# Optimization experiments

Measured on AMD Instinct MI355X. Metric: run time of the kernel, lower is better.

## Reference

```python
import jax, jax.numpy as jnp
import numpy as np

NHEADS = 16
LN_EPS = 1e-5


def setup_inputs() -> dict:
    key = jax.random.key(0)
    ks = jax.random.split(key, 12)
    B, L, D = 8, 1024, 1024
    bound = 1.0 / np.sqrt(D)
    inp = {
        'query': jax.random.normal(ks[0], (B, L, D), jnp.float32),
        'key':   jax.random.normal(ks[1], (B, L, D), jnp.float32),
        'value': jax.random.normal(ks[2], (B, L, D), jnp.float32),
        'q_mask': jnp.ones((B, L), jnp.float32),
        'k_mask': jnp.ones((B, L), jnp.float32),
        'Wq': jax.random.uniform(ks[3], (D, D), jnp.float32, -bound, bound),
        'bq': jax.random.uniform(ks[4], (D,), jnp.float32, -bound, bound),
        'Wk': jax.random.uniform(ks[5], (D, D), jnp.float32, -bound, bound),
        'bk': jax.random.uniform(ks[6], (D,), jnp.float32, -bound, bound),
        'Wv': jax.random.uniform(ks[7], (D, D), jnp.float32, -bound, bound),
        'bv': jax.random.uniform(ks[8], (D,), jnp.float32, -bound, bound),
        'Wo': jax.random.uniform(ks[9], (D, D), jnp.float32, -bound, bound),
        'bo': jax.random.uniform(ks[10], (D,), jnp.float32, -bound, bound),
        'gamma': jnp.ones((D,), jnp.float32),
        'beta': jnp.zeros((D,), jnp.float32),
    }
    return inp


def reference(query, key, value, q_mask, k_mask, Wq, bq, Wk, bk, Wv, bv, Wo, bo, gamma, beta):
    B, L, D = query.shape
    H = NHEADS
    d = D // H
    residual = query
    # linear projections (torch Linear: x @ W.T + b)
    q = query @ Wq.T + bq
    k = key @ Wk.T + bk
    v = value @ Wv.T + bv
    # NOTE: module does a raw contiguous view [B, L, H*d] -> [B*H, L, d]
    # (NOT a transpose-based head split). Replicate exactly.
    q = q.reshape(B * H, L, d)
    k = k.reshape(B * H, L, d)
    v = v.reshape(B * H, L, d)
    # masks tiled head-major: repeat(nheads, 1) -> [H*B, L]
    qm = jnp.tile(q_mask, (H, 1))
    km = jnp.tile(k_mask, (H, 1))
    mask = qm[:, :, None] * km[:, None, :]  # [B*H, L, L] outer product
    scores = jnp.einsum('bqd,bkd->bqk', q, k) / np.sqrt(d).astype(np.float32)
    A = jnp.exp(jnp.where(mask == 0, -jnp.inf, scores))  # unstable exp, as in source
    A_sum = jnp.clip(jnp.sum(A, axis=-1, keepdims=True), 2e-15, None)
    attn = A / A_sum
    context = (attn @ v).reshape(B, L, H * d)
    out = context @ Wo.T + bo
    # dropout is identity in eval mode
    x = residual + out
    mean = jnp.mean(x, axis=-1, keepdims=True)
    var = jnp.mean(jnp.square(x - mean), axis=-1, keepdims=True)
    return (x - mean) / jnp.sqrt(var + LN_EPS) * gamma + beta
```

## Files before the change

kernel.cpp:

```cpp
#include <hip/hip_runtime.h>
#include <hip/hip_bf16.h>


typedef __bf16 bf16x8 __attribute__((ext_vector_type(8)));
typedef float  f32x4  __attribute__((ext_vector_type(4)));

#define KK 1024
#define NN 1024

union BfPack4 { __bf16 h[4]; uint2 u; };
union BfPack8 { __bf16 h[8]; uint4 u; };

__device__ __forceinline__ void lds_copy16(void* lds, const void* gsrc) {
  __builtin_amdgcn_global_load_lds(
      (__attribute__((address_space(1))) void*)(uintptr_t)gsrc,
      (__attribute__((address_space(3))) void*)(unsigned int)(uintptr_t)lds,
      16, 0, 0);
}

struct Cvt4 { const float* src[4]; __bf16* dst; };

__global__ __launch_bounds__(256) void cvt_w(Cvt4 a) {
  const int z = blockIdx.y;
  const float* s = a.src[z];
  __bf16* d = a.dst + (size_t)z * (KK * NN);
  const int i = (blockIdx.x * 256 + threadIdx.x) * 4;
  float4 f = *(const float4*)&s[i];
  BfPack4 p;
  p.h[0] = (__bf16)f.x; p.h[1] = (__bf16)f.y;
  p.h[2] = (__bf16)f.z; p.h[3] = (__bf16)f.w;
  *(uint2*)&d[i] = p.u;
}

struct Cvt3 { const float* src[3]; __bf16* dst; };

__global__ __launch_bounds__(256) void cvt_a(Cvt3 a) {
  const int z = blockIdx.y;
  const float* s = a.src[z];
  __bf16* d = a.dst + (size_t)z * ((size_t)8 << 20);
  const size_t i = ((size_t)blockIdx.x * 256 + threadIdx.x) * 8;
  float4 f0 = *(const float4*)&s[i];
  float4 f1 = *(const float4*)&s[i + 4];
  BfPack8 p;
  p.h[0] = (__bf16)f0.x; p.h[1] = (__bf16)f0.y;
  p.h[2] = (__bf16)f0.z; p.h[3] = (__bf16)f0.w;
  p.h[4] = (__bf16)f1.x; p.h[5] = (__bf16)f1.y;
  p.h[6] = (__bf16)f1.z; p.h[7] = (__bf16)f1.w;
  *(uint4*)&d[i] = p.u;
}

struct G8 {
  const __bf16* A[3];
  const __bf16* W[3];
  const float*  bias[3];
  void*         C[3];
};

#define BAR()   __builtin_amdgcn_s_barrier()
#define PRIO(x) __builtin_amdgcn_s_setprio(x)
#define WAIT_LGKM0() do { asm volatile("s_waitcnt lgkmcnt(0)" ::: "memory"); \
                          __builtin_amdgcn_sched_barrier(0); } while (0)
#define WAIT_VM4()  asm volatile("s_waitcnt vmcnt(4)" ::: "memory")
#define WAIT_VM0()  asm volatile("s_waitcnt vmcnt(0)" ::: "memory")

#define STAGE_A(buf, half, kt) do {                                          \
  lds_copy16(smem + (buf)*32768 + (half)*16384 + ldsW,                       \
             pA0[half] + (size_t)(kt)*64);                                   \
  lds_copy16(smem + (buf)*32768 + (half)*16384 + ldsW + 1024,                \
             pA1[half] + (size_t)(kt)*64); } while (0)

#define STAGE_B(buf, half, kt) do {                                          \
  lds_copy16(smem + 65536 + (buf)*32768 + (half)*16384 + ldsW,               \
             pB0[half] + (size_t)(kt)*64);                                   \
  lds_copy16(smem + 65536 + (buf)*32768 + (half)*16384 + ldsW + 1024,        \
             pB1[half] + (size_t)(kt)*64); } while (0)

#define LDA(buf, mh) do {                                                    \
  const char* _p = aSelf + (buf)*32768 + (mh)*8192;                          \
  _Pragma("unroll") for (int i_ = 0; i_ < 4; ++i_) {                         \
    af[i_][0] = *(const bf16x8*)(_p + i_*2048 + c0_);                        \
    af[i_][1] = *(const bf16x8*)(_p + i_*2048 + c1_); } } while (0)

#define LDB(buf, nh) do {                                                    \
  const char* _p = bSelf + (buf)*32768 + (nh)*4096;                          \
  _Pragma("unroll") for (int j_ = 0; j_ < 2; ++j_) {                         \
    bf[(nh)*2 + j_][0] = *(const bf16x8*)(_p + j_*2048 + c0_);               \
    bf[(nh)*2 + j_][1] = *(const bf16x8*)(_p + j_*2048 + c1_); } } while (0)

#define MM(mh, nh) do {                                                      \
  _Pragma("unroll") for (int i_ = 0; i_ < 4; ++i_)                           \
  _Pragma("unroll") for (int j_ = 0; j_ < 2; ++j_) {                         \
    acc[(mh)*4+i_][(nh)*2+j_] = __builtin_amdgcn_mfma_f32_16x16x32_bf16(     \
        af[i_][0], bf[(nh)*2+j_][0], acc[(mh)*4+i_][(nh)*2+j_], 0, 0, 0);    \
    acc[(mh)*4+i_][(nh)*2+j_] = __builtin_amdgcn_mfma_f32_16x16x32_bf16(     \
        af[i_][1], bf[(nh)*2+j_][1], acc[(mh)*4+i_][(nh)*2+j_], 0, 0, 0);    \
  } } while (0)

template <bool OUT_BF16>
__global__ __launch_bounds__(512, 2) void gemm8p(G8 args)
{
  __shared__ __align__(16) char smem[131072];
  const int z = blockIdx.z;
  const __bf16* __restrict__ A    = args.A[z];
  const __bf16* __restrict__ W    = args.W[z];
  const float*  __restrict__ bias = args.bias[z];

  const int tid = threadIdx.x;
  const int l = tid & 63, w = tid >> 6;
  const int lr = l & 15, lq = l >> 4;
  const int wr = w >> 2, wc = w & 3;

  int lin = blockIdx.y * 32 + blockIdx.x;
  lin = (lin & 7) * 16 + (lin >> 3);
  const int m0 = (lin & 31) * 256;
  const int n0 = (lin >> 5) * 256;

  const int s0 = w * 128 + l, s1 = s0 + 64;
  const int r0 = s0 >> 3, kq0 = (s0 & 7) ^ (r0 & 7);
  const int r1 = s1 >> 3, kq1 = (s1 & 7) ^ (r1 & 7);
  const __bf16* pA0[2]; const __bf16* pA1[2];
  const __bf16* pB0[2]; const __bf16* pB1[2];
  #pragma unroll
  for (int h = 0; h < 2; ++h) {
    pA0[h] = A + (size_t)(m0 + h * 128 + r0) * KK + kq0 * 8;
    pA1[h] = A + (size_t)(m0 + h * 128 + r1) * KK + kq1 * 8;
    pB0[h] = W + (size_t)(n0 + h * 128 + r0) * KK + kq0 * 8;
    pB1[h] = W + (size_t)(n0 + h * 128 + r1) * KK + kq1 * 8;
  }
  const int ldsW = w * 2048;

  const int aRow = lr * 128;
  const int c0_ = ((lq)     ^ (lr & 7)) * 16;
  const int c1_ = ((4 + lq) ^ (lr & 7)) * 16;
  const char* aSelf = smem + wr * 16384 + aRow;
  const char* bSelf = smem + 65536 + (wc >> 1) * 16384 + (wc & 1) * 8192 + aRow;

  bf16x8 af[4][2], bf[4][2];
  f32x4 acc[8][4] = {};

  STAGE_A(0, 0, 0); STAGE_A(0, 1, 0);
  STAGE_B(0, 0, 0); STAGE_B(0, 1, 0);
  STAGE_B(1, 0, 1); STAGE_B(1, 1, 1);
  WAIT_VM4();
  BAR();

  for (int it = 0; it < 8; ++it) {
    const int t2 = it * 2;
    LDA(0, 0); LDB(0, 0);
    STAGE_A(1, 0, t2 + 1);
    BAR(); WAIT_LGKM0();
    PRIO(1); MM(0, 0); PRIO(0);
    BAR();
    LDB(0, 1);
    STAGE_A(1, 1, t2 + 1);
    BAR(); WAIT_LGKM0();
    PRIO(1); MM(0, 1); PRIO(0);
    BAR();
    LDA(0, 1);
    if (it < 7) STAGE_B(0, 0, t2 + 2);
    BAR(); WAIT_LGKM0();
    PRIO(1); MM(1, 0); PRIO(0);
    BAR();
    if (it < 7) { STAGE_B(0, 1, t2 + 2); WAIT_VM4(); }
    else        { WAIT_VM0(); }
    BAR();
    PRIO(1); MM(1, 1); PRIO(0);
    BAR();
    LDA(1, 0); LDB(1, 0);
    if (it < 7) STAGE_A(0, 0, t2 + 2);
    BAR(); WAIT_LGKM0();
    PRIO(1); MM(0, 0); PRIO(0);
    BAR();
    LDB(1, 1);
    if (it < 7) STAGE_A(0, 1, t2 + 2);
    BAR(); WAIT_LGKM0();
    PRIO(1); MM(0, 1); PRIO(0);
    BAR();
    LDA(1, 1);
    if (it < 7) STAGE_B(1, 0, t2 + 3);
    BAR(); WAIT_LGKM0();
    PRIO(1); MM(1, 0); PRIO(0);
    BAR();
    if (it < 7) { STAGE_B(1, 1, t2 + 3); WAIT_VM4(); }
    BAR();
    PRIO(1); MM(1, 1); PRIO(0);
    BAR();
  }

  float bv[4];
  #pragma unroll
  for (int n = 0; n < 4; ++n) bv[n] = bias[n0 + wc * 64 + n * 16 + lr];

  #pragma unroll
  for (int f = 0; f < 8; ++f) {
    const int gm = m0 + wr * 128 + f * 16 + lq * 4;
    #pragma unroll
    for (int n = 0; n < 4; ++n) {
      const int gn = n0 + wc * 64 + n * 16 + lr;
      #pragma unroll
      for (int i = 0; i < 4; ++i) {
        const float v = acc[f][n][i] + bv[n];
        if constexpr (OUT_BF16)
          ((__bf16*)args.C[z])[(size_t)(gm + i) * NN + gn] = (__bf16)v;
        else
          ((float*)args.C[z])[(size_t)(gm + i) * NN + gn] = v;
      }
    }
  }
}

struct GQKV {
  const float*  A[3];
  const __bf16* W;
  const float*  bias[3];
  __bf16*       C[3];
};

__global__ __launch_bounds__(256) void gemm_qkv(GQKV args)
{
  __shared__ alignas(16) __bf16 As[128 * 40];
  __shared__ alignas(16) __bf16 Bs[2][4096];
  const int z = blockIdx.z;
  const float*  A    = args.A[z];
  const __bf16* W    = args.W + (size_t)z * KK * NN;
  const float*  bias = args.bias[z];
  __bf16* C = args.C[z];
  const int tid = threadIdx.x, l = tid & 63, w = tid >> 6;
  const int m0 = blockIdx.x * 128, n0 = blockIdx.y * 128;
  const int lr = l & 15, lq = l >> 4;
  const int wm = (w & 1) * 64, wn = (w >> 1) * 64;

  const __bf16* gw0 = &W[(size_t)(n0 + (tid >> 2)) * KK + (tid & 3) * 8];
  const __bf16* gw1 = &W[(size_t)(n0 + 64 + (tid >> 2)) * KK + (tid & 3) * 8];

  float4 pa[4];
  #pragma unroll
  for (int s = 0; s < 4; ++s) {
    int c = tid + 256 * s; int row = c >> 3, ko = (c & 7) * 4;
    pa[s] = *(const float4*)&A[(size_t)(m0 + row) * KK + ko];
  }
  lds_copy16((char*)Bs + w * 1024,        gw0);
  lds_copy16((char*)Bs + 4096 + w * 1024, gw1);

  f32x4 acc[4][4] = {};
  int ib = 0;
  for (int kk = 0; kk < KK; kk += 32) {
    __syncthreads();
    #pragma unroll
    for (int s = 0; s < 4; ++s) {
      int c = tid + 256 * s; int row = c >> 3, ko = (c & 7) * 4;
      BfPack4 p;
      p.h[0] = (__bf16)pa[s].x; p.h[1] = (__bf16)pa[s].y;
      p.h[2] = (__bf16)pa[s].z; p.h[3] = (__bf16)pa[s].w;
      *(uint2*)&As[row * 40 + ko] = p.u;
    }
    __syncthreads();
    if (kk + 32 < KK) {
      lds_copy16((char*)Bs + (ib ^ 1) * 8192 + w * 1024,        gw0 + kk + 32);
      lds_copy16((char*)Bs + (ib ^ 1) * 8192 + 4096 + w * 1024, gw1 + kk + 32);
      #pragma unroll
      for (int s = 0; s < 4; ++s) {
        int c = tid + 256 * s; int row = c >> 3, ko = (c & 7) * 4;
        pa[s] = *(const float4*)&A[(size_t)(m0 + row) * KK + kk + 32 + ko];
      }
    }
    const __bf16* Bb = (const __bf16*)((char*)Bs + ib * 8192);
    bf16x8 af2[4], bf2[4];
    #pragma unroll
    for (int t = 0; t < 4; ++t) {
      af2[t] = *(const bf16x8*)&As[(wm + t * 16 + lr) * 40 + lq * 8];
      bf2[t] = *(const bf16x8*)&Bb[(wn + t * 16 + lr) * 32 + lq * 8];
    }
    #pragma unroll
    for (int mt = 0; mt < 4; ++mt)
      #pragma unroll
      for (int nt = 0; nt < 4; ++nt)
        acc[mt][nt] = __builtin_amdgcn_mfma_f32_16x16x32_bf16(af2[mt], bf2[nt], acc[mt][nt], 0, 0, 0);
    ib ^= 1;
  }

  #pragma unroll
  for (int mt = 0; mt < 4; ++mt)
    #pragma unroll
    for (int nt = 0; nt < 4; ++nt)
      #pragma unroll
      for (int i = 0; i < 4; ++i) {
        int gm = m0 + wm + mt * 16 + lq * 4 + i;
        int gn = n0 + wn + nt * 16 + lr;
        C[(size_t)gm * NN + gn] = (__bf16)(acc[mt][nt][i] + bias[gn]);
      }
}

__global__ __launch_bounds__(256) void attn_kernel(
    const __bf16* __restrict__ qb, const __bf16* __restrict__ kb,
    const __bf16* __restrict__ vb, const float* __restrict__ qm,
    const float* __restrict__ km, __bf16* __restrict__ ctxb)
{
  const int g  = blockIdx.y;
  const int qt = blockIdx.x;
  const int tid = threadIdx.x, l = tid & 63, w = tid >> 6;
  const int lr = l & 15, lq = l >> 4;

  __shared__ alignas(16) __bf16 Ps[128 * 72];
  __shared__ alignas(16) __bf16 Ks[2 * 128 * 32];
  __shared__ alignas(16) __bf16 Vt[64 * 136];
  __shared__ alignas(16) __bf16 kms[1024];

  const size_t gbase = (size_t)g * (1024 * 64);
  const __bf16* qg = qb + gbase;
  const __bf16* kg = kb + gbase;
  const __bf16* vg = vb + gbase;
  const float* qmrow = qm + (size_t)(g & 7) * 1024;
  const float* kmrow = km + (size_t)(g & 7) * 1024;

  #pragma unroll
  for (int s = 0; s < 4; ++s) {
    int c = tid + 256 * s;
    int p = c >> 9, r = (c >> 2) & 127, q0 = c & 3;
    lds_copy16((char*)Ps + w * 1024 + s * 4096,
               &qg[(size_t)(qt * 128 + r) * 64 + p * 32 + q0 * 8]);
  }
  {
    float4 kf = *(const float4*)&kmrow[tid * 4];
    BfPack4 p;
    p.h[0] = (__bf16)(kf.x == 0.f ? 0.f : 1.f);
    p.h[1] = (__bf16)(kf.y == 0.f ? 0.f : 1.f);
    p.h[2] = (__bf16)(kf.z == 0.f ? 0.f : 1.f);
    p.h[3] = (__bf16)(kf.w == 0.f ? 0.f : 1.f);
    *(uint2*)&kms[tid * 4] = p.u;
  }
  float qmv[2][4];
  #pragma unroll
  for (int rt = 0; rt < 2; ++rt)
    #pragma unroll
    for (int i = 0; i < 4; ++i)
      qmv[rt][i] = qmrow[qt * 128 + 32 * w + rt * 16 + lq * 4 + i];

  __syncthreads();

  bf16x8 qa[2][2];
  #pragma unroll
  for (int rt = 0; rt < 2; ++rt)
    #pragma unroll
    for (int p = 0; p < 2; ++p)
      qa[rt][p] = *(const bf16x8*)((char*)Ps + p * 8192 +
                                   (32 * w + rt * 16 + lr) * 64 + lq * 16);

  uint4 pv[4];
  #pragma unroll
  for (int s = 0; s < 4; ++s) {
    int ch = tid + 256 * s; int j = ch & 127, cc0 = ch >> 7;
    pv[s] = *(const uint4*)&vg[(size_t)j * 64 + cc0 * 8];
  }

  float rs[2][4] = {};
  f32x4 ctx[2][4] = {};

  for (int kt = 0; kt < 8; ++kt) {
    __syncthreads();
    #pragma unroll
    for (int s = 0; s < 4; ++s) {
      int c = tid + 256 * s;
      int p = c >> 9, r = (c >> 2) & 127, q0 = c & 3;
      lds_copy16((char*)Ks + w * 1024 + s * 4096,
                 &kg[(size_t)(kt * 128 + r) * 64 + p * 32 + q0 * 8]);
    }
    #pragma unroll
    for (int s = 0; s < 4; ++s) {
      int ch = tid + 256 * s; int j = ch & 127, cc0 = ch >> 7;
      BfPack8 vv; vv.u = pv[s];
      #pragma unroll
      for (int cc = 0; cc < 8; ++cc)
        Vt[(cc0 * 8 + cc) * 136 + j] = vv.h[cc];
    }
    __syncthreads();
    if (kt < 7) {
      #pragma unroll
      for (int s = 0; s < 4; ++s) {
        int ch = tid + 256 * s; int j = ch & 127, cc0 = ch >> 7;
        pv[s] = *(const uint4*)&vg[(size_t)((kt + 1) * 128 + j) * 64 + cc0 * 8];
      }
    }
    const int wkey = 16 * (lq >> 1);
    const int rkey = 16 * ((lr >> 3) & 1);
    #pragma unroll
    for (int h = 0; h < 2; ++h) {
      f32x4 sacc[2][4];
      #pragma unroll
      for (int c4 = 0; c4 < 4; ++c4) {
        int ct = h * 4 + c4;
        bf16x8 kb0 = *(const bf16x8*)((char*)Ks + (ct * 16 + lr) * 64 + lq * 16);
        bf16x8 kb1 = *(const bf16x8*)((char*)Ks + 8192 + (ct * 16 + lr) * 64 + lq * 16);
        #pragma unroll
        for (int rt = 0; rt < 2; ++rt) {
          f32x4 zz = {};
          zz = __builtin_amdgcn_mfma_f32_16x16x32_bf16(qa[rt][0], kb0, zz, 0, 0, 0);
          sacc[rt][c4] = __builtin_amdgcn_mfma_f32_16x16x32_bf16(qa[rt][1], kb1, zz, 0, 0, 0);
        }
      }
      #pragma unroll
      for (int c4 = 0; c4 < 4; ++c4) {
        int ct = h * 4 + c4;
        float kmv = (float)kms[kt * 128 + ct * 16 + lr];
        #pragma unroll
        for (int rt = 0; rt < 2; ++rt)
          #pragma unroll
          for (int i = 0; i < 4; ++i) {
            float e = (qmv[rt][i] * kmv == 0.f) ? 0.f
                                                : __expf(sacc[rt][c4][i] * 0.125f);
            rs[rt][i] += e;
            int row = 32 * w + rt * 16 + lq * 4 + i;
            Ps[row * 72 + ((c4 * 16 + lr) ^ wkey)] = (__bf16)e;
          }
      }
      #pragma unroll
      for (int ks = 0; ks < 2; ++ks) {
        bf16x8 pa2[2];
        #pragma unroll
        for (int rt = 0; rt < 2; ++rt)
          pa2[rt] = *(const bf16x8*)&Ps[(32 * w + rt * 16 + lr) * 72 +
                                        ((ks * 32 + lq * 8) ^ rkey)];
        #pragma unroll
        for (int c2 = 0; c2 < 4; ++c2) {
          bf16x8 vf = *(const bf16x8*)&Vt[(c2 * 16 + lr) * 136 +
                                          h * 64 + ks * 32 + lq * 8];
          #pragma unroll
          for (int rt = 0; rt < 2; ++rt)
            ctx[rt][c2] = __builtin_amdgcn_mfma_f32_16x16x32_bf16(pa2[rt], vf, ctx[rt][c2], 0, 0, 0);
        }
      }
    }
  }

  #pragma unroll
  for (int rt = 0; rt < 2; ++rt)
    #pragma unroll
    for (int i = 0; i < 4; ++i) {
      float v = rs[rt][i];
      v += __shfl_xor(v, 1);
      v += __shfl_xor(v, 2);
      v += __shfl_xor(v, 4);
      v += __shfl_xor(v, 8);
      rs[rt][i] = 1.0f / fmaxf(v, 2e-15f);
    }

  #pragma unroll
  for (int rt = 0; rt < 2; ++rt)
    #pragma unroll
    for (int c2 = 0; c2 < 4; ++c2)
      #pragma unroll
      for (int i = 0; i < 4; ++i) {
        int row = qt * 128 + 32 * w + rt * 16 + lq * 4 + i;
        ctxb[gbase + (size_t)row * 64 + c2 * 16 + lr] =
            (__bf16)(ctx[rt][c2][i] * rs[rt][i]);
      }
}

__global__ __launch_bounds__(256) void ln_kernel(
    const float* __restrict__ O, const float* __restrict__ resid,
    const float* __restrict__ gam, const float* __restrict__ bet,
    float* __restrict__ out)
{
  const int row = blockIdx.x;
  const int tid = threadIdx.x;
  const float* orow = O + (size_t)row * 1024;
  const float* rrow = resid + (size_t)row * 1024;
  float x[4];
  float sum = 0.f, sq = 0.f;
  #pragma unroll
  for (int j = 0; j < 4; ++j) {
    int c = tid + j * 256;
    x[j] = orow[c] + rrow[c];
    sum += x[j];
    sq  += x[j] * x[j];
  }
  #pragma unroll
  for (int off = 32; off > 0; off >>= 1) {
    sum += __shfl_down(sum, off, 64);
    sq  += __shfl_down(sq, off, 64);
  }
  __shared__ float s1[4], s2[4];
  __shared__ float mean_s, inv_s;
  if ((tid & 63) == 0) { s1[tid >> 6] = sum; s2[tid >> 6] = sq; }
  __syncthreads();
  if (tid == 0) {
    float S = s1[0] + s1[1] + s1[2] + s1[3];
    float Q = s2[0] + s2[1] + s2[2] + s2[3];
    float mean = S * (1.0f / 1024.0f);
    float var  = fmaxf(Q * (1.0f / 1024.0f) - mean * mean, 0.0f);
    mean_s = mean;
    inv_s  = rsqrtf(var + 1e-5f);
  }
  __syncthreads();
  float mean = mean_s, inv = inv_s;
  #pragma unroll
  for (int j = 0; j < 4; ++j) {
    int c = tid + j * 256;
    out[(size_t)row * 1024 + c] = (x[j] - mean) * inv * gam[c] + bet[c];
  }
}

extern "C" void kernel_launch(void* const* d_in, const int* in_sizes, int n_in,
                              void* d_out, int out_size, void* d_ws, size_t ws_size,
                              hipStream_t stream)
{
  const float* query = (const float*)d_in[0];
  const float* keyi  = (const float*)d_in[1];
  const float* value = (const float*)d_in[2];
  const float* qmask = (const float*)d_in[3];
  const float* kmask = (const float*)d_in[4];
  const float* Wq = (const float*)d_in[5];
  const float* bq = (const float*)d_in[6];
  const float* Wk = (const float*)d_in[7];
  const float* bk = (const float*)d_in[8];
  const float* Wv = (const float*)d_in[9];
  const float* bv = (const float*)d_in[10];
  const float* Wo = (const float*)d_in[11];
  const float* bo = (const float*)d_in[12];
  const float* gam = (const float*)d_in[13];
  const float* bet = (const float*)d_in[14];

  char* ws = (char*)d_ws;
  __bf16* qbuf = (__bf16*)(ws);
  __bf16* kbuf = (__bf16*)(ws + ((size_t)16 << 20));
  __bf16* vbuf = (__bf16*)(ws + ((size_t)32 << 20));
  __bf16* wb   = (__bf16*)(ws + ((size_t)48 << 20));
  float*  obuf = (float*)(ws + ((size_t)16 << 20));
  __bf16* abuf = (__bf16*)(ws + ((size_t)56 << 20));

  const bool big = ws_size >= ((size_t)104 << 20);

  Cvt4 cv;
  cv.src[0] = Wq; cv.src[1] = Wk; cv.src[2] = Wv; cv.src[3] = Wo;
  cv.dst = wb;

  dim3 tb(256);
  hipLaunchKernelGGL(cvt_w, dim3(1024, 4), tb, 0, stream, cv);

  if (big) {
    Cvt3 ca;
    ca.src[0] = query; ca.src[1] = keyi; ca.src[2] = value;
    ca.dst = abuf;
    hipLaunchKernelGGL(cvt_a, dim3(4096, 3), tb, 0, stream, ca);

    G8 gq;
    gq.A[0] = abuf;
    gq.A[1] = abuf + ((size_t)8 << 20);
    gq.A[2] = abuf + ((size_t)16 << 20);
    gq.W[0] = wb; gq.W[1] = wb + (size_t)KK * NN; gq.W[2] = wb + (size_t)2 * KK * NN;
    gq.bias[0] = bq; gq.bias[1] = bk; gq.bias[2] = bv;
    gq.C[0] = qbuf; gq.C[1] = kbuf; gq.C[2] = vbuf;
    hipLaunchKernelGGL((gemm8p<true>), dim3(32, 4, 3), dim3(512), 0, stream, gq);
  } else {
    GQKV qkv;
    qkv.A[0] = query; qkv.A[1] = keyi; qkv.A[2] = value;
    qkv.W = wb;
    qkv.bias[0] = bq; qkv.bias[1] = bk; qkv.bias[2] = bv;
    qkv.C[0] = qbuf;  qkv.C[1] = kbuf; qkv.C[2] = vbuf;
    hipLaunchKernelGGL(gemm_qkv, dim3(64, 8, 3), tb, 0, stream, qkv);
  }

  hipLaunchKernelGGL(attn_kernel, dim3(8, 128), tb, 0, stream,
                     qbuf, kbuf, vbuf, qmask, kmask, qbuf);

  G8 go;
  go.A[0] = qbuf;
  go.W[0] = wb + (size_t)3 * KK * NN;
  go.bias[0] = bo;
  go.C[0] = obuf;
  go.A[1] = go.A[2] = go.A[0]; go.W[1] = go.W[2] = go.W[0];
  go.bias[1] = go.bias[2] = go.bias[0]; go.C[1] = go.C[2] = go.C[0];
  hipLaunchKernelGGL((gemm8p<false>), dim3(32, 4, 1), dim3(512), 0, stream, go);

  hipLaunchKernelGGL(ln_kernel, dim3(8192), tb, 0, stream,
                     obuf, query, gam, bet, (float*)d_out);
}
```

Measured before the change: 387.6 us.

## Swizzle attention LDS layouts, register-prefetch K, and remap block grid

```diff
diff --git a/kernel.cpp b/kernel.cpp
--- a/kernel.cpp
+++ b/kernel.cpp
@@ -291,19 +291,19 @@
       }
 }
 
-__global__ __launch_bounds__(256) void attn_kernel(
+__global__ __launch_bounds__(256, 3) void attn_kernel(
     const __bf16* __restrict__ qb, const __bf16* __restrict__ kb,
     const __bf16* __restrict__ vb, const float* __restrict__ qm,
     const float* __restrict__ km, __bf16* __restrict__ ctxb)
 {
-  const int g  = blockIdx.y;
-  const int qt = blockIdx.x;
+  const int g  = blockIdx.x * 16 + (blockIdx.y >> 3);
+  const int qt = blockIdx.y & 7;
   const int tid = threadIdx.x, l = tid & 63, w = tid >> 6;
   const int lr = l & 15, lq = l >> 4;
 
-  __shared__ alignas(16) __bf16 Ps[128 * 72];
+  __shared__ alignas(16) __bf16 Ps[128 * 64];
   __shared__ alignas(16) __bf16 Ks[2 * 128 * 32];
-  __shared__ alignas(16) __bf16 Vt[64 * 136];
+  __shared__ alignas(16) __bf16 Vt[64 * 128];
   __shared__ alignas(16) __bf16 kms[1024];
 
   const size_t gbase = (size_t)g * (1024 * 64);
@@ -346,13 +346,19 @@
       qa[rt][p] = *(const bf16x8*)((char*)Ps + p * 8192 +
                                    (32 * w + rt * 16 + lr) * 64 + lq * 16);
 
-  uint4 pv[4];
+  uint4 pk[4], pv[4];
   #pragma unroll
   for (int s = 0; s < 4; ++s) {
-    int ch = tid + 256 * s; int j = ch & 127, cc0 = ch >> 7;
-    pv[s] = *(const uint4*)&vg[(size_t)j * 64 + cc0 * 8];
-  }
-
+    int c = tid + 256 * s; int p = c >> 9, r = (c >> 2) & 127, q0 = c & 3;
+    pk[s] = *(const uint4*)&kg[(size_t)r * 64 + p * 32 + q0 * 8];
+  }
+  #pragma unroll
+  for (int s = 0; s < 4; ++s) {
+    int ch = tid + 256 * s; int j = ch & 127, c0 = ch >> 7;
+    pv[s] = *(const uint4*)&vg[(size_t)j * 64 + c0 * 8];
+  }
+
+  const int kKey = (lq ^ (lr & 3)) << 4;
   float rs[2][4] = {};
   f32x4 ctx[2][4] = {};
 
@@ -360,37 +366,42 @@
     __syncthreads();
     #pragma unroll
     for (int s = 0; s < 4; ++s) {
-      int c = tid + 256 * s;
-      int p = c >> 9, r = (c >> 2) & 127, q0 = c & 3;
-      lds_copy16((char*)Ks + w * 1024 + s * 4096,
-                 &kg[(size_t)(kt * 128 + r) * 64 + p * 32 + q0 * 8]);
+      int c = tid + 256 * s; int p = c >> 9, r = (c >> 2) & 127, q0 = c & 3;
+      *(uint4*)((char*)Ks + p * 8192 + r * 64 + ((q0 ^ (r & 3)) << 4)) = pk[s];
     }
     #pragma unroll
     for (int s = 0; s < 4; ++s) {
-      int ch = tid + 256 * s; int j = ch & 127, cc0 = ch >> 7;
+      int ch = tid + 256 * s; int j = ch & 127, c0 = ch >> 7;
       BfPack8 vv; vv.u = pv[s];
-      #pragma unroll
-      for (int cc = 0; cc < 8; ++cc)
-        Vt[(cc0 * 8 + cc) * 136 + j] = vv.h[cc];
+      const int jhi = (j >> 3) << 4, jlo = (j & 7) * 2;
+      #pragma unroll
+      for (int cc = 0; cc < 8; ++cc) {
+        int row = c0 * 8 + cc;
+        *(__bf16*)((char*)Vt + row * 256 + (jhi ^ ((row & 15) << 4)) + jlo) =
+            vv.h[cc];
+      }
     }
     __syncthreads();
     if (kt < 7) {
       #pragma unroll
       for (int s = 0; s < 4; ++s) {
-        int ch = tid + 256 * s; int j = ch & 127, cc0 = ch >> 7;
-        pv[s] = *(const uint4*)&vg[(size_t)((kt + 1) * 128 + j) * 64 + cc0 * 8];
-      }
-    }
-    const int wkey = 16 * (lq >> 1);
-    const int rkey = 16 * ((lr >> 3) & 1);
+        int c = tid + 256 * s; int p = c >> 9, r = (c >> 2) & 127, q0 = c & 3;
+        pk[s] = *(const uint4*)&kg[(size_t)((kt + 1) * 128 + r) * 64 + p * 32 + q0 * 8];
+      }
+      #pragma unroll
+      for (int s = 0; s < 4; ++s) {
+        int ch = tid + 256 * s; int j = ch & 127, c0 = ch >> 7;
+        pv[s] = *(const uint4*)&vg[(size_t)((kt + 1) * 128 + j) * 64 + c0 * 8];
+      }
+    }
     #pragma unroll
     for (int h = 0; h < 2; ++h) {
       f32x4 sacc[2][4];
       #pragma unroll
       for (int c4 = 0; c4 < 4; ++c4) {
         int ct = h * 4 + c4;
-        bf16x8 kb0 = *(const bf16x8*)((char*)Ks + (ct * 16 + lr) * 64 + lq * 16);
-        bf16x8 kb1 = *(const bf16x8*)((char*)Ks + 8192 + (ct * 16 + lr) * 64 + lq * 16);
+        bf16x8 kb0 = *(const bf16x8*)((char*)Ks + (ct * 16 + lr) * 64 + kKey);
+        bf16x8 kb1 = *(const bf16x8*)((char*)Ks + 8192 + (ct * 16 + lr) * 64 + kKey);
         #pragma unroll
         for (int rt = 0; rt < 2; ++rt) {
           f32x4 zz = {};
@@ -410,20 +421,25 @@
                                                 : __expf(sacc[rt][c4][i] * 0.125f);
             rs[rt][i] += e;
             int row = 32 * w + rt * 16 + lq * 4 + i;
-            Ps[row * 72 + ((c4 * 16 + lr) ^ wkey)] = (__bf16)e;
+            *(__bf16*)((char*)Ps + row * 128 +
+                       (((c4 * 2 + (lr >> 3)) ^ (row & 7)) << 4) +
+                       (lr & 7) * 2) = (__bf16)e;
           }
       }
       #pragma unroll
       for (int ks = 0; ks < 2; ++ks) {
         bf16x8 pa2[2];
         #pragma unroll
-        for (int rt = 0; rt < 2; ++rt)
-          pa2[rt] = *(const bf16x8*)&Ps[(32 * w + rt * 16 + lr) * 72 +
-                                        ((ks * 32 + lq * 8) ^ rkey)];
+        for (int rt = 0; rt < 2; ++rt) {
+          int row = 32 * w + rt * 16 + lr;
+          pa2[rt] = *(const bf16x8*)((char*)Ps + row * 128 +
+                                     (((ks * 4 + lq) ^ (row & 7)) << 4));
+        }
         #pragma unroll
         for (int c2 = 0; c2 < 4; ++c2) {
-          bf16x8 vf = *(const bf16x8*)&Vt[(c2 * 16 + lr) * 136 +
-                                          h * 64 + ks * 32 + lq * 8];
+          int vrow = c2 * 16 + lr;
+          bf16x8 vf = *(const bf16x8*)((char*)Vt + vrow * 256 +
+                        (((h * 8 + ks * 4 + lq) << 4) ^ ((vrow & 15) << 4)));
           #pragma unroll
           for (int rt = 0; rt < 2; ++rt)
             ctx[rt][c2] = __builtin_amdgcn_mfma_f32_16x16x32_bf16(pa2[rt], vf, ctx[rt][c2], 0, 0, 0);
```

New measurement: 652.7 us. 68.4% more time.
